# Performance work log

Measured on AMD Instinct MI355X. Metric: run time of the kernel, lower is better.

The kernel has to match this reference:

```python
import jax, jax.numpy as jnp
import numpy as np

H, DH, ITERS, EPS, LN_EPS = 8, 32, 3, 1e-8, 1e-5

def _ln(x, w, b):
    m = jnp.mean(x, axis=-1, keepdims=True)
    v = jnp.mean(jnp.square(x - m), axis=-1, keepdims=True)
    return (x - m) * jax.lax.rsqrt(v + LN_EPS) * w + b

def setup_inputs() -> dict:
    key = jax.random.key(0)
    ks = jax.random.split(key, 16)
    B, N, D, S = 64, 4096, 256, 8
    DI = H * DH  # 256
    HID = max(D, 128)
    s = 0.02
    return {
        "inputs": jax.random.normal(ks[0], (B, N, D), jnp.float32),
        "noise": jax.random.normal(ks[1], (B, S, D), jnp.float32),
        "slots_mean": jax.random.normal(ks[2], (1, 1, D), jnp.float32),
        "slots_logvar": jax.random.normal(ks[3], (1, 1, D), jnp.float32) * s,
        "wq": jax.random.normal(ks[4], (D, DI), jnp.float32) * s,
        "bq": jnp.zeros((DI,), jnp.float32),
        "wk": jax.random.normal(ks[5], (D, DI), jnp.float32) * s,
        "bk": jnp.zeros((DI,), jnp.float32),
        "wv": jax.random.normal(ks[6], (D, DI), jnp.float32) * s,
        "bv": jnp.zeros((DI,), jnp.float32),
        "wo": jax.random.normal(ks[7], (DI, D), jnp.float32) * s,
        "bo": jnp.zeros((D,), jnp.float32),
        "w_ih": jax.random.normal(ks[8], (D, 3 * D), jnp.float32) * s,
        "b_ih": jnp.zeros((3 * D,), jnp.float32),
        "w_hh": jax.random.normal(ks[9], (D, 3 * D), jnp.float32) * s,
        "b_hh": jnp.zeros((3 * D,), jnp.float32),
        "w1": jax.random.normal(ks[10], (D, HID), jnp.float32) * s,
        "b1": jnp.zeros((HID,), jnp.float32),
        "w2": jax.random.normal(ks[11], (HID, D), jnp.float32) * s,
        "b2": jnp.zeros((D,), jnp.float32),
        "ln_in_w": jnp.ones((D,), jnp.float32), "ln_in_b": jnp.zeros((D,), jnp.float32),
        "ln_s_w": jnp.ones((D,), jnp.float32), "ln_s_b": jnp.zeros((D,), jnp.float32),
        "ln_ff_w": jnp.ones((D,), jnp.float32), "ln_ff_b": jnp.zeros((D,), jnp.float32),
    }

def reference(inputs, noise, slots_mean, slots_logvar, wq, bq, wk, bk, wv, bv,
              wo, bo, w_ih, b_ih, w_hh, b_hh, w1, b1, w2, b2,
              ln_in_w, ln_in_b, ln_s_w, ln_s_b, ln_ff_w, ln_ff_b):
    B, N, D = inputs.shape
    S = noise.shape[1]
    scale = D ** -0.5  # note: scale uses dim, per original code
    # slot init: mean + exp(logvar) * noise (faithful: exp(logvar) used directly)
    slots = slots_mean + jnp.exp(slots_logvar) * noise  # [B,S,D]
    x = _ln(inputs, ln_in_w, ln_in_b)
    k = (x @ wk + bk).reshape(B, N, H, DH).transpose(0, 2, 1, 3)  # [B,H,N,Dh]
    v = (x @ wv + bv).reshape(B, N, H, DH).transpose(0, 2, 1, 3)
    attn = None
    for _ in range(ITERS):
        slots_prev = slots
        s = _ln(slots, ln_s_w, ln_s_b)
        q = (s @ wq + bq).reshape(B, S, H, DH).transpose(0, 2, 1, 3)  # [B,H,S,Dh]
        dots = jnp.einsum('bhid,bhjd->bhij', q, k) * scale  # [B,H,S,N]
        attn = jax.nn.softmax(dots, axis=-2)  # softmax over slot axis
        attn = attn + EPS
        attn = attn / jnp.clip(jnp.sum(attn, axis=-1, keepdims=True), 1e-12)  # L1 over inputs
        upd = jnp.einsum('bhjd,bhij->bhid', v, attn)  # [B,H,S,Dh]
        upd = upd.transpose(0, 2, 1, 3).reshape(B, S, H * DH) @ wo + bo  # [B,S,D]
        # GRUCell (torch gate order r,z,n)
        xg = upd.reshape(B * S, D) @ w_ih + b_ih
        hg = slots_prev.reshape(B * S, D) @ w_hh + b_hh
        xr, xz, xn = jnp.split(xg, 3, axis=-1)
        hr, hz, hn = jnp.split(hg, 3, axis=-1)
        r = jax.nn.sigmoid(xr + hr)
        z = jax.nn.sigmoid(xz + hz)
        n = jnp.tanh(xn + r * hn)
        slots = ((1.0 - z) * n + z * slots_prev.reshape(B * S, D)).reshape(B, S, D)
        ff = _ln(slots, ln_ff_w, ln_ff_b)
        slots = slots + (jax.nn.relu(ff @ w1 + b1) @ w2 + b2)
    return slots, attn
```

## Files before the change

kernel.cpp:

```cpp
#include <hip/hip_runtime.h>
#include <stdint.h>

typedef __attribute__((ext_vector_type(8))) short bf16x8;
typedef __attribute__((ext_vector_type(4))) float f32x4;

__device__ __forceinline__ float b2f(unsigned short s) {
    unsigned int u = ((unsigned int)s) << 16;
    return __builtin_bit_cast(float, u);
}
__device__ __forceinline__ unsigned short f2b(float f) {
    unsigned int u = __builtin_bit_cast(unsigned int, f);
    u += 0x7FFFu + ((u >> 16) & 1u);
    return (unsigned short)(u >> 16);
}

#define EPS_ATTN 1e-8f
#define LN_EPS 1e-5f
#define SCALE 0.0625f

__global__ __launch_bounds__(256) void k_prep(const float* __restrict__ wk,
                                              const float* __restrict__ wv,
                                              unsigned short* __restrict__ W3) {
    int g = blockIdx.x * 256 + threadIdx.x;
    int j = g & 7;
    int f = (g >> 3) & 1023;
    int stage = g >> 13;
    int p = f & 15, qq = (f >> 4) & 3, ntl = f >> 6;
    int kc = stage >> 1, half_ = stage & 1;
    int k = kc * 32 + qq * 8 + j;
    int n = half_ * 256 + ntl * 16 + p;
    float v = (n < 256) ? wk[k * 256 + n] : wv[k * 256 + (n - 256)];
    W3[g] = f2b(v);
}

__global__ __launch_bounds__(256) void k_init(const float* __restrict__ sm,
                                              const float* __restrict__ slv,
                                              const float* __restrict__ noise,
                                              float* __restrict__ slots) {
    int idx = blockIdx.x * 256 + threadIdx.x;
    int d = idx & 255;
    slots[idx] = sm[d] + expf(slv[d]) * noise[idx];
}

__global__ __launch_bounds__(256, 2) void k_kv(
    const float* __restrict__ x, const float* __restrict__ lnw, const float* __restrict__ lnb,
    const unsigned short* __restrict__ W3, const float* __restrict__ bk, const float* __restrict__ bv,
    unsigned short* __restrict__ Kb, unsigned short* __restrict__ Vb) {
    __shared__ __align__(16) unsigned short sh[33792];
    unsigned short* As   = sh;
    unsigned short* repV = sh + 16384;
    float* bL = (float*)(sh + 32768);
    int t = threadIdx.x;
    int w = t >> 6, lane = t & 63;
    int p = lane & 15, q = lane >> 4;

    if (t < 128) {
        float4 bb = (t < 64) ? ((const float4*)bk)[t] : ((const float4*)bv)[t - 64];
        *(float4*)&bL[t * 4] = bb;
    }

    float4 lw  = ((const float4*)lnw)[lane];
    float4 lbv = ((const float4*)lnb)[lane];
    float4 xv[16];
    const float* xbase = x + ((size_t)blockIdx.x * 64 + w * 16) * 256;
    #pragma unroll
    for (int i = 0; i < 16; ++i) xv[i] = ((const float4*)(xbase + i * 256))[lane];
    int kcw = lane >> 3, qw = (lane >> 1) & 3, j0 = (lane & 1) * 4;
    #pragma unroll
    for (int i = 0; i < 16; ++i) {
        float4 v = xv[i];
        float s0 = v.x + v.y + v.z + v.w;
        float s1 = v.x * v.x + v.y * v.y + v.z * v.z + v.w * v.w;
        #pragma unroll
        for (int o = 1; o < 64; o <<= 1) { s0 += __shfl_xor(s0, o); s1 += __shfl_xor(s1, o); }
        float mean = s0 * (1.0f / 256.0f);
        float var  = s1 * (1.0f / 256.0f) - mean * mean;
        float rstd = rsqrtf(var + LN_EPS);
        ushort4 pk;
        pk.x = f2b((v.x - mean) * rstd * lw.x + lbv.x);
        pk.y = f2b((v.y - mean) * rstd * lw.y + lbv.y);
        pk.z = f2b((v.z - mean) * rstd * lw.z + lbv.z);
        pk.w = f2b((v.w - mean) * rstd * lw.w + lbv.w);
        int pos = (qw * 16 + i) ^ kcw;
        *(ushort4*)&As[((w * 8 + kcw) * 64 + pos) * 8 + j0] = pk;
    }
    __syncthreads();

    f32x4 acc[4][8];
    f32x4 zero = {0.f, 0.f, 0.f, 0.f};
    #pragma unroll
    for (int rt = 0; rt < 4; ++rt)
        #pragma unroll
        for (int ct = 0; ct < 8; ++ct) acc[rt][ct] = zero;

    const unsigned short* Wb = W3 + (size_t)(w >> 1) * 8192 + (size_t)((w & 1) * 8) * 512 + lane * 8;
    #pragma unroll 2
    for (int kc = 0; kc < 8; ++kc) {
        bf16x8 af[4];
        #pragma unroll
        for (int rt = 0; rt < 4; ++rt)
            af[rt] = *(const bf16x8*)&As[((rt * 8 + kc) * 64 + ((q * 16 + p) ^ kc)) * 8];
        #pragma unroll
        for (int ct = 0; ct < 8; ++ct) {
            bf16x8 bf = *(const bf16x8*)(Wb + (size_t)kc * 16384 + ct * 512);
            #pragma unroll
            for (int rt = 0; rt < 4; ++rt)
                acc[rt][ct] = __builtin_amdgcn_mfma_f32_16x16x32_bf16(af[rt], bf, acc[rt][ct], 0, 0, 0);
        }
    }
    __syncthreads();

    unsigned short* repK = As;
    int b_  = blockIdx.x >> 6;
    int n0g = (blockIdx.x & 63) * 64;

    if (w < 2) {
        #pragma unroll
        for (int ct = 0; ct < 8; ++ct) {
            int col = w * 128 + ct * 16 + p;
            float bias = bL[col];
            int hl = col >> 5, dh = col & 31;
            #pragma unroll
            for (int rt = 0; rt < 4; ++rt) {
                #pragma unroll
                for (int r = 0; r < 4; ++r) {
                    int nl = rt * 16 + q * 4 + r;
                    repK[(hl * 64 + nl) * 32 + dh] = f2b(acc[rt][ct][r] + bias);
                }
            }
        }
    } else {
        #pragma unroll
        for (int ct = 0; ct < 8; ++ct) {
            int vrow = (w - 2) * 128 + ct * 16 + p;
            float bias = bL[256 + vrow];
            #pragma unroll
            for (int rt = 0; rt < 4; ++rt) {
                int chunk = (rt * 4 + q) ^ (p & 14);
                ushort4 pk;
                pk.x = f2b(acc[rt][ct][0] + bias);
                pk.y = f2b(acc[rt][ct][1] + bias);
                pk.z = f2b(acc[rt][ct][2] + bias);
                pk.w = f2b(acc[rt][ct][3] + bias);
                *(ushort4*)&repV[vrow * 64 + chunk * 4] = pk;
            }
        }
    }
    __syncthreads();

    #pragma unroll
    for (int i = 0; i < 8; ++i) {
        uint4 vd = *(const uint4*)&repK[(i * 256 + t) * 8];
        *(uint4*)(Kb + (((size_t)b_ * 8 + i) * 4096 + n0g) * 32 + t * 8) = vd;
    }
    #pragma unroll
    for (int i = 0; i < 8; ++i) {
        int vrow = i * 32 + (t >> 3);
        int c16 = t & 7;
        uint4 vd = *(const uint4*)&repV[vrow * 64 + ((2 * c16) ^ (vrow & 14)) * 4];
        *(uint4*)(Vb + ((size_t)(b_ * 8 + (vrow >> 5)) * 32 + (vrow & 31)) * 4096 + n0g + c16 * 8) = vd;
    }
}

__global__ __launch_bounds__(256) void k_q(
    const float* __restrict__ slots, const float* __restrict__ lnw, const float* __restrict__ lnb,
    const float* __restrict__ wq, const float* __restrict__ bq, float* __restrict__ qg) {
    __shared__ float sln[256];
    __shared__ float red[8];
    int t = threadIdx.x;
    int row = blockIdx.x;
    float v = slots[(size_t)row * 256 + t];
    float s0 = v, s1 = v * v;
    #pragma unroll
    for (int off = 1; off < 64; off <<= 1) { s0 += __shfl_xor(s0, off); s1 += __shfl_xor(s1, off); }
    if ((t & 63) == 0) { red[t >> 6] = s0; red[4 + (t >> 6)] = s1; }
    __syncthreads();
    float ts0 = red[0] + red[1] + red[2] + red[3];
    float ts1 = red[4] + red[5] + red[6] + red[7];
    float mean = ts0 * (1.f / 256.f);
    float var  = ts1 * (1.f / 256.f) - mean * mean;
    float rstd = rsqrtf(var + LN_EPS);
    sln[t] = (v - mean) * rstd * lnw[t] + lnb[t];
    __syncthreads();
    float acc = bq[t];
    #pragma unroll 4
    for (int k = 0; k < 256; ++k) acc += sln[k] * wq[k * 256 + t];
    int b = row >> 3, sl = row & 7;
    qg[(size_t)b * 2048 + (t >> 5) * 256 + sl * 32 + (t & 31)] = acc;
}

__global__ __launch_bounds__(512) void k_attn(
    const unsigned short* __restrict__ Kg, const unsigned short* __restrict__ VTg,
    const float* __restrict__ qg, float* __restrict__ upd_raw, float* __restrict__ rowsum,
    float* __restrict__ attn_out, int last) {
    __shared__ float supd[8][256];
    __shared__ float srs[8][8];
    int t = threadIdx.x;
    int w = t >> 6, lane = t & 63;
    int c = lane & 15;
    int g = lane >> 4;

    int bh = blockIdx.x;
    const unsigned short* Kbh = Kg  + (size_t)bh * 4096 * 32;
    const unsigned short* Vbh = VTg + (size_t)bh * 32 * 4096;

    bf16x8 qhi = {0,0,0,0,0,0,0,0};
    bf16x8 qlo = {0,0,0,0,0,0,0,0};
    if (c < 8) {
        const float* qp = qg + (size_t)bh * 256 + c * 32 + g * 8;
        #pragma unroll
        for (int j = 0; j < 8; ++j) {
            float qv = qp[j];
            unsigned short hb = f2b(qv);
            qhi[j] = (short)hb;
            qlo[j] = (short)f2b(qv - b2f(hb));
        }
    }

    f32x4 zero = {0.f, 0.f, 0.f, 0.f};
    f32x4 accL = zero, accH = zero;
    float rs = 0.f;
    int nb0 = w * 512;

    #pragma unroll 2
    for (int pr = 0; pr < 16; ++pr) {
        int base = nb0 + pr * 32;
        bf16x8 k0 = *(const bf16x8*)(Kbh + (size_t)(base + c) * 32 + g * 8);
        bf16x8 k1 = *(const bf16x8*)(Kbh + (size_t)(base + 16 + c) * 32 + g * 8);
        const unsigned short* vlo = Vbh + (size_t)c * 4096 + base + g * 4;
        const unsigned short* vhi = Vbh + (size_t)(c + 16) * 4096 + base + g * 4;
        union { ushort4 h[2]; bf16x8 v; } V0, V1;
        V0.h[0] = *(const ushort4*)vlo;
        V0.h[1] = *(const ushort4*)(vlo + 16);
        V1.h[0] = *(const ushort4*)vhi;
        V1.h[1] = *(const ushort4*)(vhi + 16);

        f32x4 s0 = __builtin_amdgcn_mfma_f32_16x16x32_bf16(k0, qhi, zero, 0, 0, 0);
        s0 = __builtin_amdgcn_mfma_f32_16x16x32_bf16(k0, qlo, s0, 0, 0, 0);
        f32x4 s1 = __builtin_amdgcn_mfma_f32_16x16x32_bf16(k1, qhi, zero, 0, 0, 0);
        s1 = __builtin_amdgcn_mfma_f32_16x16x32_bf16(k1, qlo, s1, 0, 0, 0);

        float d0[4], d1[4];
        #pragma unroll
        for (int r = 0; r < 4; ++r) { d0[r] = s0[r] * SCALE; d1[r] = s1[r] * SCALE; }
        float m = fmaxf(fmaxf(fmaxf(d0[0], d0[1]), fmaxf(d0[2], d0[3])),
                        fmaxf(fmaxf(d1[0], d1[1]), fmaxf(d1[2], d1[3])));
        m = fmaxf(m, __shfl_xor(m, 1));
        m = fmaxf(m, __shfl_xor(m, 2));
        m = fmaxf(m, __shfl_xor(m, 4));
        m = fmaxf(m, __shfl_xor(m, 8));
        float a0[4], a1[4];
        #pragma unroll
        for (int r = 0; r < 4; ++r) {
            float e0 = __expf(d0[r] - m);
            float e1 = __expf(d1[r] - m);
            float t0 = e0;
            t0 += __shfl_xor(t0, 1); t0 += __shfl_xor(t0, 2); t0 += __shfl_xor(t0, 4);
            float t1 = e1;
            t1 += __shfl_xor(t1, 1); t1 += __shfl_xor(t1, 2); t1 += __shfl_xor(t1, 4);
            a0[r] = e0 * (1.0f / t0) + EPS_ATTN;
            a1[r] = e1 * (1.0f / t1) + EPS_ATTN;
            rs += a0[r] + a1[r];
        }
        if (last && c < 8) {
            float4 st0 = {a0[0], a0[1], a0[2], a0[3]};
            float4 st1 = {a1[0], a1[1], a1[2], a1[3]};
            float* ap = attn_out + ((size_t)bh * 8 + c) * 4096 + base + g * 4;
            *(float4*)ap = st0;
            *(float4*)(ap + 16) = st1;
        }
        bf16x8 pah, pal;
        float af[8] = {a0[0], a0[1], a0[2], a0[3], a1[0], a1[1], a1[2], a1[3]};
        #pragma unroll
        for (int j = 0; j < 8; ++j) {
            unsigned short hb = f2b(af[j]);
            pah[j] = (short)hb;
            pal[j] = (short)f2b(af[j] - b2f(hb));
        }
        accL = __builtin_amdgcn_mfma_f32_16x16x32_bf16(V0.v, pah, accL, 0, 0, 0);
        accL = __builtin_amdgcn_mfma_f32_16x16x32_bf16(V0.v, pal, accL, 0, 0, 0);
        accH = __builtin_amdgcn_mfma_f32_16x16x32_bf16(V1.v, pah, accH, 0, 0, 0);
        accH = __builtin_amdgcn_mfma_f32_16x16x32_bf16(V1.v, pal, accH, 0, 0, 0);
    }

    rs += __shfl_xor(rs, 16);
    rs += __shfl_xor(rs, 32);
    if (lane < 8) srs[w][lane] = rs;
    if (c < 8) {
        float* up = &supd[w][c * 32 + g * 4];
        up[0]  = accL[0]; up[1]  = accL[1]; up[2]  = accL[2]; up[3]  = accL[3];
        up[16] = accH[0]; up[17] = accH[1]; up[18] = accH[2]; up[19] = accH[3];
    }
    __syncthreads();
    if (t < 256) {
        float v = 0.f;
        #pragma unroll
        for (int ww = 0; ww < 8; ++ww) v += supd[ww][t];
        upd_raw[(size_t)bh * 256 + t] = v;
    }
    if (t < 8) {
        float v = 0.f;
        #pragma unroll
        for (int ww = 0; ww < 8; ++ww) v += srs[ww][t];
        rowsum[bh * 8 + t] = v;
    }
}

__global__ __launch_bounds__(256) void k_gA(
    const float* __restrict__ upd_raw, const float* __restrict__ rowsum,
    const float* __restrict__ wo, const float* __restrict__ bo, float* __restrict__ O) {
    __shared__ float Ul[8][256];
    __shared__ float Pp[4][8][64];
    int t = threadIdx.x;
    int b = blockIdx.x >> 2, cc = blockIdx.x & 3;
    int colbase = cc * 64;
    {
        int r = t >> 5, d0 = (t & 31) * 8;
        int h = d0 >> 5;
        float inv = 1.0f / fmaxf(rowsum[(b * 8 + h) * 8 + r], 1e-12f);
        const float* up = upd_raw + (size_t)(b * 8 + h) * 256 + r * 32 + (d0 & 31);
        float4 u0 = *(const float4*)up;
        float4 u1 = *(const float4*)(up + 4);
        Ul[r][d0 + 0] = u0.x * inv; Ul[r][d0 + 1] = u0.y * inv;
        Ul[r][d0 + 2] = u0.z * inv; Ul[r][d0 + 3] = u0.w * inv;
        Ul[r][d0 + 4] = u1.x * inv; Ul[r][d0 + 5] = u1.y * inv;
        Ul[r][d0 + 6] = u1.z * inv; Ul[r][d0 + 7] = u1.w * inv;
    }
    __syncthreads();
    int c = t & 63, kq = t >> 6;
    float acc[8] = {0.f,0.f,0.f,0.f,0.f,0.f,0.f,0.f};
    const float* wp = wo + (size_t)(kq * 64) * 256 + colbase + c;
    #pragma unroll 16
    for (int k = 0; k < 64; ++k) {
        float wv_ = wp[(size_t)k * 256];
        int kk = kq * 64 + k;
        #pragma unroll
        for (int r = 0; r < 8; ++r) acc[r] += Ul[r][kk] * wv_;
    }
    #pragma unroll
    for (int r = 0; r < 8; ++r) Pp[kq][r][c] = acc[r];
    __syncthreads();
    #pragma unroll
    for (int j = 0; j < 2; ++j) {
        int o = t * 2 + j;
        int r = o >> 6, c2 = o & 63;
        float v = Pp[0][r][c2] + Pp[1][r][c2] + Pp[2][r][c2] + Pp[3][r][c2] + bo[colbase + c2];
        O[(size_t)(b * 8 + r) * 256 + colbase + c2] = v;
    }
}

__global__ __launch_bounds__(256) void k_gB(
    const float* __restrict__ O, const float* __restrict__ slin,
    const float* __restrict__ wih, const float* __restrict__ bih,
    const float* __restrict__ whh, const float* __restrict__ bhh,
    float* __restrict__ gcomb, float* __restrict__ xn, float* __restrict__ hn) {
    __shared__ float Ol[8][256], Hl[8][256];
    __shared__ float Px[2][8][128], Ph[2][8][128];
    int t = threadIdx.x;
    int b = blockIdx.x / 6, cc = blockIdx.x % 6;
    int colbase = cc * 128;
    {
        int r = t >> 5, d0 = (t & 31) * 8;
        const float* op = O + (size_t)(b * 8 + r) * 256 + d0;
        const float* hp = slin + (size_t)(b * 8 + r) * 256 + d0;
        *(float4*)&Ol[r][d0]     = *(const float4*)op;
        *(float4*)&Ol[r][d0 + 4] = *(const float4*)(op + 4);
        *(float4*)&Hl[r][d0]     = *(const float4*)hp;
        *(float4*)&Hl[r][d0 + 4] = *(const float4*)(hp + 4);
    }
    __syncthreads();
    int c = t & 127, kh = t >> 7;
    float ax[8] = {0.f,0.f,0.f,0.f,0.f,0.f,0.f,0.f};
    float ah[8] = {0.f,0.f,0.f,0.f,0.f,0.f,0.f,0.f};
    const float* wxp = wih + (size_t)(kh * 128) * 768 + colbase + c;
    const float* whp = whh + (size_t)(kh * 128) * 768 + colbase + c;
    #pragma unroll 8
    for (int k = 0; k < 128; ++k) {
        float wx = wxp[(size_t)k * 768];
        float wh = whp[(size_t)k * 768];
        int kk = kh * 128 + k;
        #pragma unroll
        for (int r = 0; r < 8; ++r) { ax[r] += Ol[r][kk] * wx; ah[r] += Hl[r][kk] * wh; }
    }
    #pragma unroll
    for (int r = 0; r < 8; ++r) { Px[kh][r][c] = ax[r]; Ph[kh][r][c] = ah[r]; }
    __syncthreads();
    #pragma unroll
    for (int j = 0; j < 4; ++j) {
        int o = t * 4 + j;
        int r = o >> 7, c2 = o & 127;
        int cg = colbase + c2;
        int row = b * 8 + r;
        float vx = Px[0][r][c2] + Px[1][r][c2] + bih[cg];
        float vh = Ph[0][r][c2] + Ph[1][r][c2] + bhh[cg];
        if (cg < 512) {
            gcomb[(size_t)row * 512 + cg] = vx + vh;
        } else {
            xn[(size_t)row * 256 + cg - 512] = vx;
            hn[(size_t)row * 256 + cg - 512] = vh;
        }
    }
}

__global__ __launch_bounds__(256) void k_gC(
    const float* __restrict__ gcomb, const float* __restrict__ xn, const float* __restrict__ hn,
    const float* __restrict__ slin, const float* __restrict__ lnfw, const float* __restrict__ lnfb,
    float* __restrict__ slout, float* __restrict__ F) {
    __shared__ float red[8];
    int t = threadIdx.x, row = blockIdx.x;
    float a_r = gcomb[(size_t)row * 512 + t];
    float a_z = gcomb[(size_t)row * 512 + 256 + t];
    float xnv = xn[(size_t)row * 256 + t];
    float hnv = hn[(size_t)row * 256 + t];
    float hp  = slin[(size_t)row * 256 + t];
    float rg = 1.f / (1.f + expf(-a_r));
    float zg = 1.f / (1.f + expf(-a_z));
    float ng = tanhf(xnv + rg * hnv);
    float s1 = (1.f - zg) * ng + zg * hp;
    slout[(size_t)row * 256 + t] = s1;
    float s0 = s1, sq = s1 * s1;
    #pragma unroll
    for (int o = 1; o < 64; o <<= 1) { s0 += __shfl_xor(s0, o); sq += __shfl_xor(sq, o); }
    if ((t & 63) == 0) { red[t >> 6] = s0; red[4 + (t >> 6)] = sq; }
    __syncthreads();
    float ts0 = red[0] + red[1] + red[2] + red[3];
    float ts1 = red[4] + red[5] + red[6] + red[7];
    float mean = ts0 * (1.f / 256.f);
    float var  = ts1 * (1.f / 256.f) - mean * mean;
    float rstd = rsqrtf(var + LN_EPS);
    F[(size_t)row * 256 + t] = (s1 - mean) * rstd * lnfw[t] + lnfb[t];
}

__global__ __launch_bounds__(256) void k_gD(
    const float* __restrict__ F, const float* __restrict__ w1, const float* __restrict__ b1,
    float* __restrict__ H1) {
    __shared__ float Fl[8][256];
    __shared__ float Pp[4][8][64];
    int t = threadIdx.x;
    int b = blockIdx.x >> 2, cc = blockIdx.x & 3;
    int colbase = cc * 64;
    {
        int r = t >> 5, d0 = (t & 31) * 8;
        const float* fp = F + (size_t)(b * 8 + r) * 256 + d0;
        *(float4*)&Fl[r][d0]     = *(const float4*)fp;
        *(float4*)&Fl[r][d0 + 4] = *(const float4*)(fp + 4);
    }
    __syncthreads();
    int c = t & 63, kq = t >> 6;
    float acc[8] = {0.f,0.f,0.f,0.f,0.f,0.f,0.f,0.f};
    const float* wp = w1 + (size_t)(kq * 64) * 256 + colbase + c;
    #pragma unroll 16
    for (int k = 0; k < 64; ++k) {
        float wv_ = wp[(size_t)k * 256];
        int kk = kq * 64 + k;
        #pragma unroll
        for (int r = 0; r < 8; ++r) acc[r] += Fl[r][kk] * wv_;
    }
    #pragma unroll
    for (int r = 0; r < 8; ++r) Pp[kq][r][c] = acc[r];
    __syncthreads();
    #pragma unroll
    for (int j = 0; j < 2; ++j) {
        int o = t * 2 + j;
        int r = o >> 6, c2 = o & 63;
        float v = Pp[0][r][c2] + Pp[1][r][c2] + Pp[2][r][c2] + Pp[3][r][c2] + b1[colbase + c2];
        H1[(size_t)(b * 8 + r) * 256 + colbase + c2] = fmaxf(v, 0.f);
    }
}

__global__ __launch_bounds__(256) void k_gE(
    const float* __restrict__ H1, const float* __restrict__ w2, const float* __restrict__ b2,
    float* __restrict__ slout) {
    __shared__ float Hl[8][256];
    __shared__ float Pp[4][8][64];
    int t = threadIdx.x;
    int b = blockIdx.x >> 2, cc = blockIdx.x & 3;
    int colbase = cc * 64;
    {
        int r = t >> 5, d0 = (t & 31) * 8;
        const float* hp = H1 + (size_t)(b * 8 + r) * 256 + d0;
        *(float4*)&Hl[r][d0]     = *(const float4*)hp;
        *(float4*)&Hl[r][d0 + 4] = *(const float4*)(hp + 4);
    }
    __syncthreads();
    int c = t & 63, kq = t >> 6;
    float acc[8] = {0.f,0.f,0.f,0.f,0.f,0.f,0.f,0.f};
    const float* wp = w2 + (size_t)(kq * 64) * 256 + colbase + c;
    #pragma unroll 16
    for (int k = 0; k < 64; ++k) {
        float wv_ = wp[(size_t)k * 256];
        int kk = kq * 64 + k;
        #pragma unroll
        for (int r = 0; r < 8; ++r) acc[r] += Hl[r][kk] * wv_;
    }
    #pragma unroll
    for (int r = 0; r < 8; ++r) Pp[kq][r][c] = acc[r];
    __syncthreads();
    #pragma unroll
    for (int j = 0; j < 2; ++j) {
        int o = t * 2 + j;
        int r = o >> 6, c2 = o & 63;
        size_t idx = (size_t)(b * 8 + r) * 256 + colbase + c2;
        float v = Pp[0][r][c2] + Pp[1][r][c2] + Pp[2][r][c2] + Pp[3][r][c2] + b2[colbase + c2];
        slout[idx] = slout[idx] + v;
    }
}

__global__ __launch_bounds__(256) void k_scale(float* __restrict__ attn, const float* __restrict__ rowsum) {
    size_t i4 = ((size_t)blockIdx.x * 256 + threadIdx.x) * 4;
    int row = (int)(i4 >> 12);
    float inv = 1.0f / fmaxf(rowsum[row], 1e-12f);
    float4 v = *(float4*)(attn + i4);
    v.x *= inv; v.y *= inv; v.z *= inv; v.w *= inv;
    *(float4*)(attn + i4) = v;
}

extern "C" void kernel_launch(void* const* d_in, const int* in_sizes, int n_in,
                              void* d_out, int out_size, void* d_ws, size_t ws_size,
                              hipStream_t stream) {
    const float* inputs = (const float*)d_in[0];
    const float* noise  = (const float*)d_in[1];
    const float* sm     = (const float*)d_in[2];
    const float* slv    = (const float*)d_in[3];
    const float* wq     = (const float*)d_in[4];
    const float* bq     = (const float*)d_in[5];
    const float* wk     = (const float*)d_in[6];
    const float* bk     = (const float*)d_in[7];
    const float* wv     = (const float*)d_in[8];
    const float* bv     = (const float*)d_in[9];
    const float* wo     = (const float*)d_in[10];
    const float* bo     = (const float*)d_in[11];
    const float* wih    = (const float*)d_in[12];
    const float* bih    = (const float*)d_in[13];
    const float* whh    = (const float*)d_in[14];
    const float* bhh    = (const float*)d_in[15];
    const float* w1     = (const float*)d_in[16];
    const float* b1     = (const float*)d_in[17];
    const float* w2     = (const float*)d_in[18];
    const float* b2     = (const float*)d_in[19];
    const float* lniw   = (const float*)d_in[20];
    const float* lnib   = (const float*)d_in[21];
    const float* lnsw   = (const float*)d_in[22];
    const float* lnsb   = (const float*)d_in[23];
    const float* lnfw   = (const float*)d_in[24];
    const float* lnfb   = (const float*)d_in[25];

    char* ws = (char*)d_ws;
    unsigned short* Kb = (unsigned short*)ws;
    unsigned short* Vb = (unsigned short*)(ws + 134217728ull);
    float* slotsA  = (float*)(ws + 268435456ull);
    float* slotsB  = (float*)(ws + 268959744ull);
    float* Rr      = (float*)(ws + 269484032ull);
    float* Pr      = (float*)(ws + 270008320ull);
    float* Qr      = (float*)(ws + 270532608ull);
    float* upd_raw = (float*)(ws + 272629760ull);
    float* rowsum  = (float*)(ws + 273154048ull);
    unsigned short* W3 = (unsigned short*)Pr;
    float* O_  = Pr;
    float* gcomb = Qr;
    float* xn = Qr + 262144;
    float* hn = Qr + 393216;
    float* H1 = Qr;
    float* qg = Rr;
    float* F_ = Rr;

    float* out_slots = (float*)d_out;
    float* attn_out  = (float*)d_out + 131072;

    k_prep<<<512, 256, 0, stream>>>(wk, wv, W3);
    k_init<<<512, 256, 0, stream>>>(sm, slv, noise, slotsA);
    k_kv<<<4096, 256, 0, stream>>>(inputs, lniw, lnib, W3, bk, bv, Kb, Vb);
    for (int it = 0; it < 3; ++it) {
        int last = (it == 2);
        float* sl_in  = (it == 0) ? slotsA : ((it == 1) ? slotsB : slotsA);
        float* sl_out = (it == 0) ? slotsB : ((it == 1) ? slotsA : out_slots);
        k_q<<<512, 256, 0, stream>>>(sl_in, lnsw, lnsb, wq, bq, qg);
        k_attn<<<512, 512, 0, stream>>>(Kb, Vb, qg, upd_raw, rowsum, attn_out, last);
        k_gA<<<256, 256, 0, stream>>>(upd_raw, rowsum, wo, bo, O_);
        k_gB<<<384, 256, 0, stream>>>(O_, sl_in, wih, bih, whh, bhh, gcomb, xn, hn);
        k_gC<<<512, 256, 0, stream>>>(gcomb, xn, hn, sl_in, lnfw, lnfb, sl_out, F_);
        k_gD<<<256, 256, 0, stream>>>(F_, w1, b1, H1);
        k_gE<<<256, 256, 0, stream>>>(H1, w2, b2, sl_out);
    }
    k_scale<<<16384, 256, 0, stream>>>(attn_out, rowsum);
}
```

Before: 1.068 ms.

## Split attention over N into four chunks and halve k_kv shared memory

k_attn now runs four 256-thread blocks per (batch, head), each covering a quarter of the inputs. It writes partial updates and row sums that k_gA reduces, and k_gA also saves total row sums for the final scaling pass. k_kv reuses a single shared staging buffer for K and then V, with an extra barrier in between. This halves its LDS use so the launch bound can allow four blocks per CU. The aim is more parallelism and occupancy for the two heavy kernels, at the cost of partial-sum traffic and extra synchronisation.

```diff
diff --git a/kernel.cpp b/kernel.cpp
--- a/kernel.cpp
+++ b/kernel.cpp
@@ -42,14 +42,13 @@
     slots[idx] = sm[d] + expf(slv[d]) * noise[idx];
 }
 
-__global__ __launch_bounds__(256, 2) void k_kv(
+__global__ __launch_bounds__(256, 4) void k_kv(
     const float* __restrict__ x, const float* __restrict__ lnw, const float* __restrict__ lnb,
     const unsigned short* __restrict__ W3, const float* __restrict__ bk, const float* __restrict__ bv,
     unsigned short* __restrict__ Kb, unsigned short* __restrict__ Vb) {
-    __shared__ __align__(16) unsigned short sh[33792];
-    unsigned short* As   = sh;
-    unsigned short* repV = sh + 16384;
-    float* bL = (float*)(sh + 32768);
+    __shared__ __align__(16) unsigned short sh[16384];
+    __shared__ __align__(16) float bL[512];
+    unsigned short* As = sh;
     int t = threadIdx.x;
     int w = t >> 6, lane = t & 63;
     int p = lane & 15, q = lane >> 4;
@@ -110,7 +109,7 @@
     }
     __syncthreads();
 
-    unsigned short* repK = As;
+    unsigned short* rep = As;
     int b_  = blockIdx.x >> 6;
     int n0g = (blockIdx.x & 63) * 64;
 
@@ -125,11 +124,20 @@
                 #pragma unroll
                 for (int r = 0; r < 4; ++r) {
                     int nl = rt * 16 + q * 4 + r;
-                    repK[(hl * 64 + nl) * 32 + dh] = f2b(acc[rt][ct][r] + bias);
+                    rep[(hl * 64 + nl) * 32 + dh] = f2b(acc[rt][ct][r] + bias);
                 }
             }
         }
-    } else {
+    }
+    __syncthreads();
+    #pragma unroll
+    for (int i = 0; i < 8; ++i) {
+        uint4 vd = *(const uint4*)&rep[(i * 256 + t) * 8];
+        *(uint4*)(Kb + (((size_t)b_ * 8 + i) * 4096 + n0g) * 32 + t * 8) = vd;
+    }
+    __syncthreads();
+
+    if (w >= 2) {
         #pragma unroll
         for (int ct = 0; ct < 8; ++ct) {
             int vrow = (w - 2) * 128 + ct * 16 + p;
@@ -142,22 +150,16 @@
                 pk.y = f2b(acc[rt][ct][1] + bias);
                 pk.z = f2b(acc[rt][ct][2] + bias);
                 pk.w = f2b(acc[rt][ct][3] + bias);
-                *(ushort4*)&repV[vrow * 64 + chunk * 4] = pk;
+                *(ushort4*)&rep[vrow * 64 + chunk * 4] = pk;
             }
         }
     }
     __syncthreads();
-
-    #pragma unroll
-    for (int i = 0; i < 8; ++i) {
-        uint4 vd = *(const uint4*)&repK[(i * 256 + t) * 8];
-        *(uint4*)(Kb + (((size_t)b_ * 8 + i) * 4096 + n0g) * 32 + t * 8) = vd;
-    }
     #pragma unroll
     for (int i = 0; i < 8; ++i) {
         int vrow = i * 32 + (t >> 3);
         int c16 = t & 7;
-        uint4 vd = *(const uint4*)&repV[vrow * 64 + ((2 * c16) ^ (vrow & 14)) * 4];
+        uint4 vd = *(const uint4*)&rep[vrow * 64 + ((2 * c16) ^ (vrow & 14)) * 4];
         *(uint4*)(Vb + ((size_t)(b_ * 8 + (vrow >> 5)) * 32 + (vrow & 31)) * 4096 + n0g + c16 * 8) = vd;
     }
 }
@@ -189,18 +191,19 @@
     qg[(size_t)b * 2048 + (t >> 5) * 256 + sl * 32 + (t & 31)] = acc;
 }
 
-__global__ __launch_bounds__(512) void k_attn(
+__global__ __launch_bounds__(256) void k_attn(
     const unsigned short* __restrict__ Kg, const unsigned short* __restrict__ VTg,
-    const float* __restrict__ qg, float* __restrict__ upd_raw, float* __restrict__ rowsum,
+    const float* __restrict__ qg, float* __restrict__ upd_part, float* __restrict__ rowsum_part,
     float* __restrict__ attn_out, int last) {
-    __shared__ float supd[8][256];
-    __shared__ float srs[8][8];
+    __shared__ float supd[4][256];
+    __shared__ float srs[4][8];
     int t = threadIdx.x;
     int w = t >> 6, lane = t & 63;
     int c = lane & 15;
     int g = lane >> 4;
 
-    int bh = blockIdx.x;
+    int bh = blockIdx.x >> 2;
+    int chunk = blockIdx.x & 3;
     const unsigned short* Kbh = Kg  + (size_t)bh * 4096 * 32;
     const unsigned short* Vbh = VTg + (size_t)bh * 32 * 4096;
 
@@ -220,10 +223,10 @@
     f32x4 zero = {0.f, 0.f, 0.f, 0.f};
     f32x4 accL = zero, accH = zero;
     float rs = 0.f;
-    int nb0 = w * 512;
+    int nb0 = chunk * 1024 + w * 256;
 
     #pragma unroll 2
-    for (int pr = 0; pr < 16; ++pr) {
+    for (int pr = 0; pr < 8; ++pr) {
         int base = nb0 + pr * 32;
         bf16x8 k0 = *(const bf16x8*)(Kbh + (size_t)(base + c) * 32 + g * 8);
         bf16x8 k1 = *(const bf16x8*)(Kbh + (size_t)(base + 16 + c) * 32 + g * 8);
@@ -292,23 +295,20 @@
         up[16] = accH[0]; up[17] = accH[1]; up[18] = accH[2]; up[19] = accH[3];
     }
     __syncthreads();
-    if (t < 256) {
-        float v = 0.f;
-        #pragma unroll
-        for (int ww = 0; ww < 8; ++ww) v += supd[ww][t];
-        upd_raw[(size_t)bh * 256 + t] = v;
+    {
+        float v = supd[0][t] + supd[1][t] + supd[2][t] + supd[3][t];
+        upd_part[((size_t)bh * 4 + chunk) * 256 + t] = v;
     }
     if (t < 8) {
-        float v = 0.f;
-        #pragma unroll
-        for (int ww = 0; ww < 8; ++ww) v += srs[ww][t];
-        rowsum[bh * 8 + t] = v;
+        float v = srs[0][t] + srs[1][t] + srs[2][t] + srs[3][t];
+        rowsum_part[((size_t)bh * 4 + chunk) * 8 + t] = v;
     }
 }
 
 __global__ __launch_bounds__(256) void k_gA(
-    const float* __restrict__ upd_raw, const float* __restrict__ rowsum,
-    const float* __restrict__ wo, const float* __restrict__ bo, float* __restrict__ O) {
+    const float* __restrict__ upd_part, const float* __restrict__ rowsum_part,
+    const float* __restrict__ wo, const float* __restrict__ bo,
+    float* __restrict__ O, float* __restrict__ rowsum_tot) {
     __shared__ float Ul[8][256];
     __shared__ float Pp[4][8][64];
     int t = threadIdx.x;
@@ -316,15 +316,24 @@
     int colbase = cc * 64;
     {
         int r = t >> 5, d0 = (t & 31) * 8;
-        int h = d0 >> 5;
-        float inv = 1.0f / fmaxf(rowsum[(b * 8 + h) * 8 + r], 1e-12f);
-        const float* up = upd_raw + (size_t)(b * 8 + h) * 256 + r * 32 + (d0 & 31);
-        float4 u0 = *(const float4*)up;
-        float4 u1 = *(const float4*)(up + 4);
-        Ul[r][d0 + 0] = u0.x * inv; Ul[r][d0 + 1] = u0.y * inv;
-        Ul[r][d0 + 2] = u0.z * inv; Ul[r][d0 + 3] = u0.w * inv;
-        Ul[r][d0 + 4] = u1.x * inv; Ul[r][d0 + 5] = u1.y * inv;
-        Ul[r][d0 + 6] = u1.z * inv; Ul[r][d0 + 7] = u1.w * inv;
+        int h = (t & 31) >> 2;
+        float rsum = 0.f;
+        #pragma unroll
+        for (int ch = 0; ch < 4; ++ch)
+            rsum += rowsum_part[((size_t)(b * 8 + h) * 4 + ch) * 8 + r];
+        float inv = 1.0f / fmaxf(rsum, 1e-12f);
+        float u[8] = {0.f,0.f,0.f,0.f,0.f,0.f,0.f,0.f};
+        #pragma unroll
+        for (int ch = 0; ch < 4; ++ch) {
+            const float* up = upd_part + ((size_t)(b * 8 + h) * 4 + ch) * 256 + r * 32 + (d0 & 31);
+            float4 u0 = *(const float4*)up;
+            float4 u1 = *(const float4*)(up + 4);
+            u[0] += u0.x; u[1] += u0.y; u[2] += u0.z; u[3] += u0.w;
+            u[4] += u1.x; u[5] += u1.y; u[6] += u1.z; u[7] += u1.w;
+        }
+        #pragma unroll
+        for (int i = 0; i < 8; ++i) Ul[r][d0 + i] = u[i] * inv;
+        if (cc == 0 && (t & 3) == 0) rowsum_tot[(b * 8 + h) * 8 + r] = rsum;
     }
     __syncthreads();
     int c = t & 63, kq = t >> 6;
@@ -506,10 +515,10 @@
     }
 }
 
-__global__ __launch_bounds__(256) void k_scale(float* __restrict__ attn, const float* __restrict__ rowsum) {
+__global__ __launch_bounds__(256) void k_scale(float* __restrict__ attn, const float* __restrict__ rowsum_tot) {
     size_t i4 = ((size_t)blockIdx.x * 256 + threadIdx.x) * 4;
     int row = (int)(i4 >> 12);
-    float inv = 1.0f / fmaxf(rowsum[row], 1e-12f);
+    float inv = 1.0f / fmaxf(rowsum_tot[row], 1e-12f);
     float4 v = *(float4*)(attn + i4);
     v.x *= inv; v.y *= inv; v.z *= inv; v.w *= inv;
     *(float4*)(attn + i4) = v;
@@ -553,10 +562,11 @@
     float* Rr      = (float*)(ws + 269484032ull);
     float* Pr      = (float*)(ws + 270008320ull);
     float* Qr      = (float*)(ws + 270532608ull);
-    float* upd_raw = (float*)(ws + 272629760ull);
-    float* rowsum  = (float*)(ws + 273154048ull);
+    float* rowsum_part = (float*)(ws + 272629760ull);
+    float* rowsum_tot  = (float*)(ws + 273154048ull);
     unsigned short* W3 = (unsigned short*)Pr;
     float* O_  = Pr;
+    float* upd_part = Qr;
     float* gcomb = Qr;
     float* xn = Qr + 262144;
     float* hn = Qr + 393216;
@@ -575,12 +585,12 @@
         float* sl_in  = (it == 0) ? slotsA : ((it == 1) ? slotsB : slotsA);
         float* sl_out = (it == 0) ? slotsB : ((it == 1) ? slotsA : out_slots);
         k_q<<<512, 256, 0, stream>>>(sl_in, lnsw, lnsb, wq, bq, qg);
-        k_attn<<<512, 512, 0, stream>>>(Kb, Vb, qg, upd_raw, rowsum, attn_out, last);
-        k_gA<<<256, 256, 0, stream>>>(upd_raw, rowsum, wo, bo, O_);
+        k_attn<<<2048, 256, 0, stream>>>(Kb, Vb, qg, upd_part, rowsum_part, attn_out, last);
+        k_gA<<<256, 256, 0, stream>>>(upd_part, rowsum_part, wo, bo, O_, rowsum_tot);
         k_gB<<<384, 256, 0, stream>>>(O_, sl_in, wih, bih, whh, bhh, gcomb, xn, hn);
         k_gC<<<512, 256, 0, stream>>>(gcomb, xn, hn, sl_in, lnfw, lnfb, sl_out, F_);
         k_gD<<<256, 256, 0, stream>>>(F_, w1, b1, H1);
         k_gE<<<256, 256, 0, stream>>>(H1, w2, b2, sl_out);
     }
-    k_scale<<<16384, 256, 0, stream>>>(attn_out, rowsum);
-}
+    k_scale<<<16384, 256, 0, stream>>>(attn_out, rowsum_tot);
+}
```

New measurement: 1.408 ms. 31.8% more time.
